# Kernel tuning notes

Hardware: AMD Instinct MI355X
Metric: run time of the kernel (lower is better)

The kernel has to match this reference:

```python
import jax, jax.numpy as jnp
import numpy as np

B, T, S, D = 8, 16, 256, 1024
H, KVH, HD = 16, 4, 64
GROUPS = H // KVH
SCALE = HD ** -0.5
CAP = 50.0
EPS = 1e-6


def setup_inputs() -> dict:
    key = jax.random.key(0)
    ks = jax.random.split(key, 5)
    return {
        "x": jax.random.normal(ks[0], (B, T, S, D), dtype=jnp.float32),
        "Wq": jax.random.normal(ks[1], (D, H * HD), dtype=jnp.float32) * (D ** -0.5),
        "Wk": jax.random.normal(ks[2], (D, KVH * HD), dtype=jnp.float32) * (D ** -0.5),
        "Wv": jax.random.normal(ks[3], (D, KVH * HD), dtype=jnp.float32) * (D ** -0.5),
        "Wo": jax.random.normal(ks[4], (H * HD, D), dtype=jnp.float32) * ((H * HD) ** -0.5),
        "q_norm_w": jnp.ones((HD,), dtype=jnp.float32),
        "k_norm_w": jnp.ones((HD,), dtype=jnp.float32),
    }


def _rmsnorm(x, w):
    rms = jnp.sqrt(jnp.mean(x * x, axis=-1, keepdims=True) + EPS)
    return x / rms * w


def reference(x, Wq, Wk, Wv, Wo, q_norm_w, k_norm_w):
    b, t, s, d = x.shape
    xf = x.reshape(b * t, s, d)                    # (BT, S, D)
    q = (xf @ Wq).reshape(b * t, s, H, HD).transpose(0, 2, 1, 3)   # (BT, H, S, hd)
    k = (xf @ Wk).reshape(b * t, s, KVH, HD).transpose(0, 2, 1, 3)  # (BT, KVH, S, hd)
    v = (xf @ Wv).reshape(b * t, s, KVH, HD).transpose(0, 2, 1, 3)
    q = _rmsnorm(q, q_norm_w)
    k = _rmsnorm(k, k_norm_w)
    if GROUPS > 1:
        k = jnp.repeat(k, GROUPS, axis=1)          # (BT, H, S, hd)
        v = jnp.repeat(v, GROUPS, axis=1)
    logits = jnp.einsum("bhqd,bhkd->bhqk", q, k) * SCALE
    logits = CAP * jnp.tanh(logits / CAP)          # soft cap
    attn = jax.nn.softmax(logits, axis=-1)
    out = jnp.einsum("bhqk,bhkd->bhqd", attn, v)   # (BT, H, S, hd)
    out = out.transpose(0, 2, 1, 3).reshape(b * t, s, H * HD)
    out = out @ Wo
    return out.reshape(b, t, s, d)
```

## Files before the change

kernel.cpp:

```cpp
#include <hip/hip_runtime.h>
#include <cstdint>
#include <cstddef>

typedef __bf16 bf16x8 __attribute__((ext_vector_type(8)));
typedef float f32x4 __attribute__((ext_vector_type(4)));
typedef unsigned short u16;
typedef unsigned int u32;
typedef unsigned short u16x8 __attribute__((ext_vector_type(8)));
typedef unsigned int u32x4v __attribute__((ext_vector_type(4)));

#define ROWS 32768
#define DMODEL 1024
#define NQKV 1536
#define C1_ 0.0072134752044448170f
#define A2_ 144.26950408889634f
#define B2_ 72.13475204444817f

__device__ __forceinline__ u16 f2bf(float f) {
    unsigned u = __float_as_uint(f);
    u += 0x7fffu + ((u >> 16) & 1u);
    return (u16)(u >> 16);
}
__device__ __forceinline__ float bf_lo(u32 u) { return __uint_as_float(u << 16); }
__device__ __forceinline__ float bf_hi(u32 u) { return __uint_as_float(u & 0xffff0000u); }
__device__ __forceinline__ u32 pack_rne(float lo, float hi) {
    return (u32)f2bf(lo) | ((u32)f2bf(hi) << 16);
}

__global__ __launch_bounds__(256) void f32_to_bf16_vec(
    const float* __restrict__ in, u16* __restrict__ out, int n4)
{
    int i = blockIdx.x * 256 + threadIdx.x;
    if (i >= n4) return;
    float4 f = ((const float4*)in)[i];
    ushort4 u;
    u.x = f2bf(f.x); u.y = f2bf(f.y); u.z = f2bf(f.z); u.w = f2bf(f.w);
    ((ushort4*)out)[i] = u;
}

__global__ __launch_bounds__(256) void transpose_bf16(
    const float* __restrict__ src, u16* __restrict__ dst, int R, int C)
{
    __shared__ float tile[32][33];
    int c0 = blockIdx.x * 32;
    int r0 = blockIdx.y * 32;
    int tx = threadIdx.x & 31;
    int ty = threadIdx.x >> 5;
#pragma unroll
    for (int i = 0; i < 32; i += 8)
        tile[ty + i][tx] = src[(size_t)(r0 + ty + i) * C + (c0 + tx)];
    __syncthreads();
#pragma unroll
    for (int i = 0; i < 32; i += 8)
        dst[(size_t)(c0 + ty + i) * R + (r0 + tx)] = f2bf(tile[tx][ty + i]);
}

template<bool BF16OUT, int NY, bool AHB>
__global__ __launch_bounds__(256) void gemm_bt(
    const u16* __restrict__ A, const u16* __restrict__ Bt,
    void* __restrict__ Cout, int M, int N, int K)
{
    __shared__ u16 As[128][32];
    __shared__ u16 Bs[128][32];
    const int tid  = threadIdx.x;
    const int wave = tid >> 6;
    const int lane = tid & 63;
    const int q4   = lane >> 4;
    const int cl   = lane & 15;
    const int wr   = wave >> 1, wc = wave & 1;
    const int id   = blockIdx.y * gridDim.x + blockIdx.x;
    const int cpx  = (gridDim.x * gridDim.y) >> 3;
    const int swz  = (id & 7) * cpx + (id >> 3);
    const int m0   = (swz / NY) * 128;
    const int n0   = (swz % NY) * 128;
    const int srow = lane >> 2;
    const int skoff = (lane & 3) * 8;

    const f32x4 zero = {0.f, 0.f, 0.f, 0.f};
    f32x4 acc[4][4];
#pragma unroll
    for (int i = 0; i < 4; ++i)
#pragma unroll
        for (int j = 0; j < 4; ++j) acc[i][j] = zero;

    for (int k0 = 0; k0 < K; k0 += 32) {
        __syncthreads();
#pragma unroll
        for (int cc = 0; cc < 2; ++cc) {
            int r = 32 * wave + 16 * cc + srow;
            const u16* ga;
            if (AHB) {
                int hh = k0 >> 6;
                ga = A + ((size_t)hh * M + (m0 + r)) * 64 + (k0 & 63) + skoff;
            } else {
                ga = A + (size_t)(m0 + r) * K + k0 + skoff;
            }
            __builtin_amdgcn_global_load_lds(
                (const __attribute__((address_space(1))) void*)ga,
                (__attribute__((address_space(3))) void*)(&As[32 * wave + 16 * cc][0]),
                16, 0, 0);
            const u16* gb = Bt + (size_t)(n0 + r) * K + k0 + skoff;
            __builtin_amdgcn_global_load_lds(
                (const __attribute__((address_space(1))) void*)gb,
                (__attribute__((address_space(3))) void*)(&Bs[32 * wave + 16 * cc][0]),
                16, 0, 0);
        }
        __syncthreads();
        bf16x8 af[4], bfr[4];
#pragma unroll
        for (int i = 0; i < 4; ++i)
            af[i] = *(const bf16x8*)&As[64 * wr + 16 * i + cl][q4 * 8];
#pragma unroll
        for (int j = 0; j < 4; ++j)
            bfr[j] = *(const bf16x8*)&Bs[64 * wc + 16 * j + cl][q4 * 8];
#pragma unroll
        for (int i = 0; i < 4; ++i)
#pragma unroll
            for (int j = 0; j < 4; ++j)
                acc[i][j] = __builtin_amdgcn_mfma_f32_16x16x32_bf16(
                    af[i], bfr[j], acc[i][j], 0, 0, 0);
    }

#pragma unroll
    for (int i = 0; i < 4; ++i)
#pragma unroll
        for (int j = 0; j < 4; ++j)
#pragma unroll
            for (int r = 0; r < 4; ++r) {
                int row = m0 + 64 * wr + 16 * i + q4 * 4 + r;
                int col = n0 + 64 * wc + 16 * j + cl;
                if (BF16OUT)
                    ((u16*)Cout)[(size_t)row * N + col] = f2bf(acc[i][j][r]);
                else
                    ((float*)Cout)[(size_t)row * N + col] = acc[i][j][r];
            }
}

__global__ __launch_bounds__(256, 3) void attention_kernel(
    const u16* __restrict__ qkv, const float* __restrict__ qw,
    const float* __restrict__ kw, u16* __restrict__ ao)
{
    const int lg  = (blockIdx.x & 7) * 256 + (blockIdx.x >> 3);
    const int bt  = lg >> 4;
    const int h   = lg & 15;
    const int kvh = h >> 2;
    const int tid  = threadIdx.x;
    const int wave = tid >> 6;
    const int lane = tid & 63;
    const int q4   = lane >> 4;
    const int cl   = lane & 15;

    __shared__ __align__(16) u16 Vt[64][264];
    __shared__ float rk_s[256];
    __shared__ float rq_s[256];

    {
        const u16* rowb = qkv + (size_t)(bt * 256 + tid) * NQKV;
        const u16* vrow = rowb + 1280 + kvh * 64;
#pragma unroll
        for (int ch = 0; ch < 8; ++ch) {
            u16x8 v8 = *(const u16x8*)(vrow + ch * 8);
#pragma unroll
            for (int e = 0; e < 8; ++e) Vt[ch * 8 + e][tid] = v8[e];
        }
        float ssk = 0.f, ssq = 0.f;
#pragma unroll
        for (int ch = 0; ch < 8; ++ch) {
            uint4 kk = *(const uint4*)(rowb + 1024 + kvh * 64 + ch * 8);
            uint4 qq = *(const uint4*)(rowb + h * 64 + ch * 8);
            const u32* uk = (const u32*)&kk;
            const u32* uq = (const u32*)&qq;
#pragma unroll
            for (int e = 0; e < 4; ++e) {
                float lo = bf_lo(uk[e]), hi = bf_hi(uk[e]);
                ssk += lo * lo + hi * hi;
                lo = bf_lo(uq[e]); hi = bf_hi(uq[e]);
                ssq += lo * lo + hi * hi;
            }
        }
        rk_s[tid] = rsqrtf(ssk * (1.0f / 64.0f) + 1e-6f) * C1_;
        rq_s[tid] = rsqrtf(ssq * (1.0f / 64.0f) + 1e-6f);
    }
    __syncthreads();

    const u16* qbase = qkv + (size_t)(bt * 256) * NQKV + h * 64;
    const u16* kbase = qkv + (size_t)(bt * 256) * NQKV + 1024 + kvh * 64;

    float wqk[2][8];
#pragma unroll
    for (int ks = 0; ks < 2; ++ks)
#pragma unroll
        for (int e = 0; e < 8; ++e) {
            int d = ks * 32 + q4 * 8 + e;
            wqk[ks][e] = qw[d] * kw[d];
        }
    uint4 qa[2][4];
#pragma unroll
    for (int i = 0; i < 4; ++i)
#pragma unroll
        for (int ks = 0; ks < 2; ++ks) {
            qa[ks][i] = *(const uint4*)(qbase +
                (size_t)(wave * 64 + 16 * i + cl) * NQKV + ks * 32 + q4 * 8);
            u32* u = (u32*)&qa[ks][i];
#pragma unroll
            for (int e = 0; e < 4; ++e) {
                float lo = bf_lo(u[e]) * wqk[ks][2 * e];
                float hi = bf_hi(u[e]) * wqk[ks][2 * e + 1];
                u[e] = pack_rne(lo, hi);
            }
        }
    float rq[4];
#pragma unroll
    for (int i = 0; i < 4; ++i)
        rq[i] = rq_s[wave * 64 + 16 * i + cl];

    const f32x4 zero = {0.f, 0.f, 0.f, 0.f};
    f32x4 o[4][4];
    float lsum[4] = {0.f, 0.f, 0.f, 0.f};
#pragma unroll
    for (int i = 0; i < 4; ++i)
#pragma unroll
        for (int j = 0; j < 4; ++j) o[i][j] = zero;

    for (int nb = 0; nb < 4; ++nb) {
#pragma unroll
        for (int jh = 0; jh < 2; ++jh) {
            const int cb = nb * 64 + jh * 32;
            float rkc[2][4];
#pragma unroll
            for (int jj = 0; jj < 2; ++jj)
#pragma unroll
                for (int r = 0; r < 4; ++r)
                    rkc[jj][r] = rk_s[cb + 16 * jj + 4 * q4 + r];
            uint4 kb[2][2];
#pragma unroll
            for (int jj = 0; jj < 2; ++jj)
#pragma unroll
                for (int ks = 0; ks < 2; ++ks)
                    kb[jj][ks] = *(const uint4*)(kbase +
                        (size_t)(cb + 16 * jj + cl) * NQKV + ks * 32 + q4 * 8);
            bf16x8 vb[4];
#pragma unroll
            for (int j2 = 0; j2 < 4; ++j2) {
                uint2 lo4 = *(const uint2*)&Vt[16 * j2 + cl][cb + 4 * q4];
                uint2 hi4 = *(const uint2*)&Vt[16 * j2 + cl][cb + 16 + 4 * q4];
                u32x4v vv = {lo4.x, lo4.y, hi4.x, hi4.y};
                vb[j2] = *(const bf16x8*)&vv;
            }
#pragma unroll
            for (int i = 0; i < 4; ++i) {
                f32x4 s0 = __builtin_amdgcn_mfma_f32_16x16x32_bf16(
                    *(const bf16x8*)&kb[0][0], *(const bf16x8*)&qa[0][i], zero, 0, 0, 0);
                s0 = __builtin_amdgcn_mfma_f32_16x16x32_bf16(
                    *(const bf16x8*)&kb[0][1], *(const bf16x8*)&qa[1][i], s0, 0, 0, 0);
                f32x4 s1 = __builtin_amdgcn_mfma_f32_16x16x32_bf16(
                    *(const bf16x8*)&kb[1][0], *(const bf16x8*)&qa[0][i], zero, 0, 0, 0);
                s1 = __builtin_amdgcn_mfma_f32_16x16x32_bf16(
                    *(const bf16x8*)&kb[1][1], *(const bf16x8*)&qa[1][i], s1, 0, 0, 0);
                float p0[4], p1[4];
#pragma unroll
                for (int r = 0; r < 4; ++r) {
                    float e2a = __builtin_amdgcn_exp2f(s0[r] * rq[i] * rkc[0][r]);
                    float rca = __builtin_amdgcn_rcpf(e2a + 1.0f);
                    p0[r] = __builtin_amdgcn_exp2f(fmaf(-A2_, rca, B2_));
                    float e2b = __builtin_amdgcn_exp2f(s1[r] * rq[i] * rkc[1][r]);
                    float rcb = __builtin_amdgcn_rcpf(e2b + 1.0f);
                    p1[r] = __builtin_amdgcn_exp2f(fmaf(-A2_, rcb, B2_));
                    lsum[i] += p0[r] + p1[r];
                }
                u32x4v paw = {pack_rne(p0[0], p0[1]), pack_rne(p0[2], p0[3]),
                              pack_rne(p1[0], p1[1]), pack_rne(p1[2], p1[3])};
                bf16x8 pa = *(const bf16x8*)&paw;
#pragma unroll
                for (int j2 = 0; j2 < 4; ++j2)
                    o[i][j2] = __builtin_amdgcn_mfma_f32_16x16x32_bf16(
                        pa, vb[j2], o[i][j2], 0, 0, 0);
            }
        }
    }

#pragma unroll
    for (int i = 0; i < 4; ++i) {
        lsum[i] += __shfl_xor(lsum[i], 16, 64);
        lsum[i] += __shfl_xor(lsum[i], 32, 64);
    }
    u16* aob = ao + ((size_t)h * ROWS + (size_t)(bt * 256 + wave * 64)) * 64;
#pragma unroll
    for (int i = 0; i < 4; ++i)
#pragma unroll
        for (int r = 0; r < 4; ++r) {
            float inv = 1.0f / __shfl(lsum[i], 4 * q4 + r, 64);
            int lr = 16 * i + 4 * q4 + r;
#pragma unroll
            for (int j = 0; j < 4; ++j)
                aob[(size_t)lr * 64 + 16 * j + cl] = f2bf(o[i][j][r] * inv);
        }
}

extern "C" void kernel_launch(void* const* d_in, const int* in_sizes, int n_in,
                              void* d_out, int out_size, void* d_ws, size_t ws_size,
                              hipStream_t stream)
{
    const float* x  = (const float*)d_in[0];
    const float* Wq = (const float*)d_in[1];
    const float* Wk = (const float*)d_in[2];
    const float* Wv = (const float*)d_in[3];
    const float* Wo = (const float*)d_in[4];
    const float* qw = (const float*)d_in[5];
    const float* kw = (const float*)d_in[6];
    float* out = (float*)d_out;

    char* ws = (char*)d_ws;
    u16* Xb  = (u16*)(ws);
    u16* QKV = (u16*)(ws + (size_t)67108864);
    u16* AO  = (u16*)(ws + (size_t)167772160);
    u16* WcT = (u16*)(ws + (size_t)234881024);
    u16* WoT = (u16*)(ws + (size_t)238026752);

    f32_to_bf16_vec<<<dim3(32768), dim3(256), 0, stream>>>(x, Xb, 8388608);
    transpose_bf16<<<dim3(32, 32), dim3(256), 0, stream>>>(Wq, WcT, 1024, 1024);
    transpose_bf16<<<dim3(8, 32), dim3(256), 0, stream>>>(Wk, WcT + (size_t)1024 * 1024, 1024, 256);
    transpose_bf16<<<dim3(8, 32), dim3(256), 0, stream>>>(Wv, WcT + (size_t)1280 * 1024, 1024, 256);
    transpose_bf16<<<dim3(32, 32), dim3(256), 0, stream>>>(Wo, WoT, 1024, 1024);
    gemm_bt<true, 12, false><<<dim3(256, 12), dim3(256), 0, stream>>>(Xb, WcT, (void*)QKV, ROWS, NQKV, 1024);
    attention_kernel<<<dim3(2048), dim3(256), 0, stream>>>(QKV, qw, kw, AO);
    gemm_bt<false, 8, true><<<dim3(256, 8), dim3(256), 0, stream>>>(AO, WoT, (void*)out, ROWS, DMODEL, 1024);
}
```

Baseline: 709.5 us.

## Split attention block across eight waves with 32 query rows each

Raises the attention block from 256 to 512 threads, so each wave handles 32 query rows instead of 64. The cooperative prologue that transposes V and computes the RMS norms is split between the two thread halves. The QK and softmax stage is reordered so the bf16 probabilities are packed per key tile before the PV MFMAs. The aim is lower per-thread register pressure and more resident waves to hide latency, at the cost of each K tile being loaded from global memory by twice as many waves.

```diff
diff --git a/kernel.cpp b/kernel.cpp
--- a/kernel.cpp
+++ b/kernel.cpp
@@ -136,7 +136,7 @@
             }
 }
 
-__global__ __launch_bounds__(256, 3) void attention_kernel(
+__global__ __launch_bounds__(512, 4) void attention_kernel(
     const u16* __restrict__ qkv, const float* __restrict__ qw,
     const float* __restrict__ kw, u16* __restrict__ ao)
 {
@@ -155,31 +155,32 @@
     __shared__ float rq_s[256];
 
     {
-        const u16* rowb = qkv + (size_t)(bt * 256 + tid) * NQKV;
-        const u16* vrow = rowb + 1280 + kvh * 64;
+        const int s  = tid >> 1;
+        const int hb = tid & 1;
+        const u16* vrow = qkv + (size_t)(bt * 256 + s) * NQKV + 1280 + kvh * 64 + hb * 32;
+#pragma unroll
+        for (int ch = 0; ch < 4; ++ch) {
+            u16x8 v8 = *(const u16x8*)(vrow + ch * 8);
+#pragma unroll
+            for (int e = 0; e < 8; ++e) Vt[hb * 32 + ch * 8 + e][s] = v8[e];
+        }
+        const int t = tid & 255;
+        const u16* rowb = qkv + (size_t)(bt * 256 + t) * NQKV;
+        const u16* src  = (tid < 256) ? (rowb + 1024 + kvh * 64) : (rowb + h * 64);
+        float ss = 0.f;
 #pragma unroll
         for (int ch = 0; ch < 8; ++ch) {
-            u16x8 v8 = *(const u16x8*)(vrow + ch * 8);
-#pragma unroll
-            for (int e = 0; e < 8; ++e) Vt[ch * 8 + e][tid] = v8[e];
-        }
-        float ssk = 0.f, ssq = 0.f;
-#pragma unroll
-        for (int ch = 0; ch < 8; ++ch) {
-            uint4 kk = *(const uint4*)(rowb + 1024 + kvh * 64 + ch * 8);
-            uint4 qq = *(const uint4*)(rowb + h * 64 + ch * 8);
+            uint4 kk = *(const uint4*)(src + ch * 8);
             const u32* uk = (const u32*)&kk;
-            const u32* uq = (const u32*)&qq;
 #pragma unroll
             for (int e = 0; e < 4; ++e) {
                 float lo = bf_lo(uk[e]), hi = bf_hi(uk[e]);
-                ssk += lo * lo + hi * hi;
-                lo = bf_lo(uq[e]); hi = bf_hi(uq[e]);
-                ssq += lo * lo + hi * hi;
-            }
-        }
-        rk_s[tid] = rsqrtf(ssk * (1.0f / 64.0f) + 1e-6f) * C1_;
-        rq_s[tid] = rsqrtf(ssq * (1.0f / 64.0f) + 1e-6f);
+                ss += lo * lo + hi * hi;
+            }
+        }
+        float rv = rsqrtf(ss * (1.0f / 64.0f) + 1e-6f);
+        if (tid < 256) rk_s[t] = rv * C1_;
+        else           rq_s[t] = rv;
     }
     __syncthreads();
 
@@ -194,13 +195,13 @@
             int d = ks * 32 + q4 * 8 + e;
             wqk[ks][e] = qw[d] * kw[d];
         }
-    uint4 qa[2][4];
-#pragma unroll
-    for (int i = 0; i < 4; ++i)
+    uint4 qa[2][2];
+#pragma unroll
+    for (int i = 0; i < 2; ++i)
 #pragma unroll
         for (int ks = 0; ks < 2; ++ks) {
             qa[ks][i] = *(const uint4*)(qbase +
-                (size_t)(wave * 64 + 16 * i + cl) * NQKV + ks * 32 + q4 * 8);
+                (size_t)(wave * 32 + 16 * i + cl) * NQKV + ks * 32 + q4 * 8);
             u32* u = (u32*)&qa[ks][i];
 #pragma unroll
             for (int e = 0; e < 4; ++e) {
@@ -209,16 +210,16 @@
                 u[e] = pack_rne(lo, hi);
             }
         }
-    float rq[4];
-#pragma unroll
-    for (int i = 0; i < 4; ++i)
-        rq[i] = rq_s[wave * 64 + 16 * i + cl];
+    float rq[2];
+#pragma unroll
+    for (int i = 0; i < 2; ++i)
+        rq[i] = rq_s[wave * 32 + 16 * i + cl];
 
     const f32x4 zero = {0.f, 0.f, 0.f, 0.f};
-    f32x4 o[4][4];
-    float lsum[4] = {0.f, 0.f, 0.f, 0.f};
-#pragma unroll
-    for (int i = 0; i < 4; ++i)
+    f32x4 o[2][4];
+    float lsum[2] = {0.f, 0.f};
+#pragma unroll
+    for (int i = 0; i < 2; ++i)
 #pragma unroll
         for (int j = 0; j < 4; ++j) o[i][j] = zero;
 
@@ -232,13 +233,31 @@
 #pragma unroll
                 for (int r = 0; r < 4; ++r)
                     rkc[jj][r] = rk_s[cb + 16 * jj + 4 * q4 + r];
-            uint4 kb[2][2];
-#pragma unroll
-            for (int jj = 0; jj < 2; ++jj)
-#pragma unroll
-                for (int ks = 0; ks < 2; ++ks)
-                    kb[jj][ks] = *(const uint4*)(kbase +
-                        (size_t)(cb + 16 * jj + cl) * NQKV + ks * 32 + q4 * 8);
+            u32 pw[2][4];
+#pragma unroll
+            for (int jj = 0; jj < 2; ++jj) {
+                uint4 kb0 = *(const uint4*)(kbase +
+                    (size_t)(cb + 16 * jj + cl) * NQKV + q4 * 8);
+                uint4 kb1 = *(const uint4*)(kbase +
+                    (size_t)(cb + 16 * jj + cl) * NQKV + 32 + q4 * 8);
+#pragma unroll
+                for (int i = 0; i < 2; ++i) {
+                    f32x4 s = __builtin_amdgcn_mfma_f32_16x16x32_bf16(
+                        *(const bf16x8*)&kb0, *(const bf16x8*)&qa[0][i], zero, 0, 0, 0);
+                    s = __builtin_amdgcn_mfma_f32_16x16x32_bf16(
+                        *(const bf16x8*)&kb1, *(const bf16x8*)&qa[1][i], s, 0, 0, 0);
+                    float p[4];
+#pragma unroll
+                    for (int r = 0; r < 4; ++r) {
+                        float e2 = __builtin_amdgcn_exp2f(s[r] * rq[i] * rkc[jj][r]);
+                        float rc = __builtin_amdgcn_rcpf(e2 + 1.0f);
+                        p[r] = __builtin_amdgcn_exp2f(fmaf(-A2_, rc, B2_));
+                    }
+                    lsum[i] += (p[0] + p[1]) + (p[2] + p[3]);
+                    pw[i][2 * jj]     = pack_rne(p[0], p[1]);
+                    pw[i][2 * jj + 1] = pack_rne(p[2], p[3]);
+                }
+            }
             bf16x8 vb[4];
 #pragma unroll
             for (int j2 = 0; j2 < 4; ++j2) {
@@ -248,28 +267,8 @@
                 vb[j2] = *(const bf16x8*)&vv;
             }
 #pragma unroll
-            for (int i = 0; i < 4; ++i) {
-                f32x4 s0 = __builtin_amdgcn_mfma_f32_16x16x32_bf16(
-                    *(const bf16x8*)&kb[0][0], *(const bf16x8*)&qa[0][i], zero, 0, 0, 0);
-                s0 = __builtin_amdgcn_mfma_f32_16x16x32_bf16(
-                    *(const bf16x8*)&kb[0][1], *(const bf16x8*)&qa[1][i], s0, 0, 0, 0);
-                f32x4 s1 = __builtin_amdgcn_mfma_f32_16x16x32_bf16(
-                    *(const bf16x8*)&kb[1][0], *(const bf16x8*)&qa[0][i], zero, 0, 0, 0);
-                s1 = __builtin_amdgcn_mfma_f32_16x16x32_bf16(
-                    *(const bf16x8*)&kb[1][1], *(const bf16x8*)&qa[1][i], s1, 0, 0, 0);
-                float p0[4], p1[4];
-#pragma unroll
-                for (int r = 0; r < 4; ++r) {
-                    float e2a = __builtin_amdgcn_exp2f(s0[r] * rq[i] * rkc[0][r]);
-                    float rca = __builtin_amdgcn_rcpf(e2a + 1.0f);
-                    p0[r] = __builtin_amdgcn_exp2f(fmaf(-A2_, rca, B2_));
-                    float e2b = __builtin_amdgcn_exp2f(s1[r] * rq[i] * rkc[1][r]);
-                    float rcb = __builtin_amdgcn_rcpf(e2b + 1.0f);
-                    p1[r] = __builtin_amdgcn_exp2f(fmaf(-A2_, rcb, B2_));
-                    lsum[i] += p0[r] + p1[r];
-                }
-                u32x4v paw = {pack_rne(p0[0], p0[1]), pack_rne(p0[2], p0[3]),
-                              pack_rne(p1[0], p1[1]), pack_rne(p1[2], p1[3])};
+            for (int i = 0; i < 2; ++i) {
+                u32x4v paw = {pw[i][0], pw[i][1], pw[i][2], pw[i][3]};
                 bf16x8 pa = *(const bf16x8*)&paw;
 #pragma unroll
                 for (int j2 = 0; j2 < 4; ++j2)
@@ -280,13 +279,13 @@
     }
 
 #pragma unroll
-    for (int i = 0; i < 4; ++i) {
+    for (int i = 0; i < 2; ++i) {
         lsum[i] += __shfl_xor(lsum[i], 16, 64);
         lsum[i] += __shfl_xor(lsum[i], 32, 64);
     }
-    u16* aob = ao + ((size_t)h * ROWS + (size_t)(bt * 256 + wave * 64)) * 64;
-#pragma unroll
-    for (int i = 0; i < 4; ++i)
+    u16* aob = ao + ((size_t)h * ROWS + (size_t)(bt * 256 + wave * 32)) * 64;
+#pragma unroll
+    for (int i = 0; i < 2; ++i)
 #pragma unroll
         for (int r = 0; r < 4; ++r) {
             float inv = 1.0f / __shfl(lsum[i], 4 * q4 + r, 64);
@@ -323,6 +322,6 @@
     transpose_bf16<<<dim3(8, 32), dim3(256), 0, stream>>>(Wv, WcT + (size_t)1280 * 1024, 1024, 256);
     transpose_bf16<<<dim3(32, 32), dim3(256), 0, stream>>>(Wo, WoT, 1024, 1024);
     gemm_bt<true, 12, false><<<dim3(256, 12), dim3(256), 0, stream>>>(Xb, WcT, (void*)QKV, ROWS, NQKV, 1024);
-    attention_kernel<<<dim3(2048), dim3(256), 0, stream>>>(QKV, qw, kw, AO);
+    attention_kernel<<<dim3(2048), dim3(512), 0, stream>>>(QKV, qw, kw, AO);
     gemm_bt<false, 8, true><<<dim3(256, 8), dim3(256), 0, stream>>>(AO, WoT, (void*)out, ROWS, DMODEL, 1024);
 }
```

New measurement: 576.4 us. -18.8%, faster.
